# Optimization experiments

Hardware: AMD Instinct MI355X
Metric: run time of the kernel (lower is better)

The kernel has to match this reference:

```python
import jax, jax.numpy as jnp
import numpy as np

V, E, H, L, B, T = 50000, 512, 512, 32, 64, 512


def _lstm_dir(xg, w_hh, reverse):
    # xg: [B,T,4H] precomputed input-to-gate projections (+ biases)
    b, t, g4 = xg.shape
    h_dim = g4 // 4
    def step(carry, xt):
        h, c = carry
        g = xt + h @ w_hh.T  # [B,4H], PyTorch gate order i,f,g,o
        i, f, gg, o = jnp.split(g, 4, axis=-1)
        c = jax.nn.sigmoid(f) * c + jax.nn.sigmoid(i) * jnp.tanh(gg)
        h = jax.nn.sigmoid(o) * jnp.tanh(c)
        return (h, c), h
    init = (jnp.zeros((b, h_dim), xg.dtype), jnp.zeros((b, h_dim), xg.dtype))
    _, hs = jax.lax.scan(step, init, jnp.swapaxes(xg, 0, 1), reverse=reverse)
    return jnp.swapaxes(hs, 0, 1)  # [B,T,H]


def _bilstm(x, w_ih0, w_ih1, w_hh, b_ih, b_hh):
    w_ihs = (w_ih0, w_ih1)
    for l in range(2):
        outs = []
        for d in range(2):  # 0=forward, 1=backward
            xg = jnp.einsum('bti,gi->btg', x, w_ihs[l][d]) + b_ih[l, d] + b_hh[l, d]
            outs.append(_lstm_dir(xg, w_hh[l, d], reverse=(d == 1)))
        x = jnp.concatenate(outs, axis=-1)  # [B,T,2H]
    return x


def _crf_nll(emissions, tags, start, end, trans):
    # pytorch-crf: returns sum log-likelihood; module returns its negation.
    emit = jnp.take_along_axis(emissions, tags[..., None], axis=-1)[..., 0]  # [B,T]
    num = (start[tags[:, 0]] + emit.sum(1)
           + trans[tags[:, :-1], tags[:, 1:]].sum(1) + end[tags[:, -1]])
    alpha0 = start + emissions[:, 0]  # [B,L]
    def step(alpha, e_t):
        s = alpha[:, :, None] + trans[None] + e_t[:, None, :]  # [B,L,L]
        return jax.nn.logsumexp(s, axis=1), None
    alpha, _ = jax.lax.scan(step, alpha0, jnp.swapaxes(emissions[:, 1:], 0, 1))
    denom = jax.nn.logsumexp(alpha + end, axis=-1)  # [B]
    return -(num - denom).sum()


def setup_inputs() -> dict:
    key = jax.random.key(0)
    ks = jax.random.split(key, 13)
    s = 0.05
    emb = jax.random.normal(ks[0], (V, E), jnp.float32) * s
    emb = emb.at[0].set(0.0)  # padding_idx=0
    return {
        'datas': jax.random.randint(ks[1], (B, T), 0, V, jnp.int32),
        'labels': jax.random.randint(ks[2], (B, T), 0, L, jnp.int32),
        'emb': emb,
        'w_ih0': jax.random.normal(ks[3], (2, 4 * H, E), jnp.float32) * s,
        'w_ih1': jax.random.normal(ks[4], (2, 4 * H, 2 * H), jnp.float32) * s,
        'w_hh': jax.random.normal(ks[5], (2, 2, 4 * H, H), jnp.float32) * s,
        'b_ih': jax.random.normal(ks[6], (2, 2, 4 * H), jnp.float32) * s,
        'b_hh': jax.random.normal(ks[7], (2, 2, 4 * H), jnp.float32) * s,
        'w_out': jax.random.normal(ks[8], (2 * H, L), jnp.float32) * s,
        'b_out': jax.random.normal(ks[9], (L,), jnp.float32) * s,
        'crf_start': jax.random.normal(ks[10], (L,), jnp.float32) * s,
        'crf_end': jax.random.normal(ks[11], (L,), jnp.float32) * s,
        'crf_trans': jax.random.normal(ks[12], (L, L), jnp.float32) * s,
    }


def reference(datas, labels, emb, w_ih0, w_ih1, w_hh, b_ih, b_hh, w_out, b_out,
              crf_start, crf_end, crf_trans):
    x = emb[datas]  # [B,T,E]
    h = _bilstm(x, w_ih0, w_ih1, w_hh, b_ih, b_hh)  # [B,T,2H]; dropout=0 (eval)
    emissions = h @ w_out + b_out  # [B,T,L]
    return _crf_nll(emissions, labels, crf_start, crf_end, crf_trans)
```

## Files before the change

### kernel.cpp

```cpp
#include <hip/hip_runtime.h>

typedef unsigned short ushort_t;
typedef unsigned long long u64_t;
typedef __attribute__((ext_vector_type(8))) short short8;
typedef __attribute__((ext_vector_type(4))) float floatx4;


__device__ __forceinline__ float bf2f(ushort_t u) {
  unsigned x = ((unsigned)u) << 16;
  return __builtin_bit_cast(float, x);
}
__device__ __forceinline__ ushort_t f2bf(float f) {
  unsigned x = __builtin_bit_cast(unsigned, f);
  x += 0x7FFFu + ((x >> 16) & 1u);
  return (ushort_t)(x >> 16);
}
__device__ __forceinline__ float sigf(float x) { return 1.0f / (1.0f + __expf(-x)); }
__device__ __forceinline__ float tanhf_(float x) { return 1.0f - 2.0f / (__expf(2.0f * x) + 1.0f); }

static const size_t OFF_A    = 0;
static const size_t OFF_OUT0 = 67108864;
static const size_t OFF_XG   = 134217728;
static const size_t OFF_WIH0 = 167772160;
static const size_t OFF_WIH1 = 171966464;
static const size_t OFF_BIAS = 180355072;
static const size_t OFF_WOUT = 180387840;
static const size_t OFF_HC   = 180453376;
static const size_t OFF_CST  = 181501952;
static const size_t OFF_BAR  = 182026240;
static const size_t OFF_NUM  = 182034432;
static const size_t OFF_PERB = 182034688;
static const size_t OFF_END  = 182034944;

__global__ void prep_kernel(const float* __restrict__ w_ih0, const float* __restrict__ w_ih1,
                            const float* __restrict__ b_ih, const float* __restrict__ b_hh,
                            const float* __restrict__ w_out,
                            ushort_t* __restrict__ wih0_bf, ushort_t* __restrict__ wih1_bf,
                            float* __restrict__ bias, ushort_t* __restrict__ wout_bf) {
  int idx = blockIdx.x * 256 + threadIdx.x;
  int stride = gridDim.x * 256;
  for (int i = idx; i < 2097152; i += stride) wih0_bf[i] = f2bf(w_ih0[i]);
  for (int i = idx; i < 4194304; i += stride) wih1_bf[i] = f2bf(w_ih1[i]);
  for (int i = idx; i < 8192; i += stride) bias[i] = b_ih[i] + b_hh[i];
  for (int i = idx; i < 32768; i += stride) {
    int j = i & 7, Ls = (i >> 3) & 63, kb = (i >> 9) & 31, nt = i >> 14;
    int n = nt * 16 + (Ls & 15);
    int k = kb * 32 + ((Ls >> 4) & 3) * 8 + j;
    wout_bf[i] = f2bf(w_out[k * 32 + n]);
  }
}

__global__ void embed_kernel(const int* __restrict__ datas, const float* __restrict__ emb,
                             ushort_t* __restrict__ x_bf) {
  int idx = blockIdx.x * 256 + threadIdx.x;
  int row = idx >> 6, sub = idx & 63;
  int tok = datas[row];
  const float4* ep = (const float4*)(emb + (size_t)tok * 512 + sub * 8);
  float4 f0 = ep[0], f1 = ep[1];
  short8 v;
  v[0] = (short)f2bf(f0.x); v[1] = (short)f2bf(f0.y);
  v[2] = (short)f2bf(f0.z); v[3] = (short)f2bf(f0.w);
  v[4] = (short)f2bf(f1.x); v[5] = (short)f2bf(f1.y);
  v[6] = (short)f2bf(f1.z); v[7] = (short)f2bf(f1.w);
  *(short8*)(x_bf + (size_t)row * 512 + sub * 8) = v;
}

__global__ __launch_bounds__(256) void gemm_chunk(const ushort_t* __restrict__ A, int K,
                                                  const ushort_t* __restrict__ W,
                                                  const float* __restrict__ biasL,
                                                  ushort_t* __restrict__ xg0c,
                                                  ushort_t* __restrict__ xg1c,
                                                  int t00, int t01) {
  __shared__ alignas(16) ushort_t alds[512 * 8];
  __shared__ alignas(16) ushort_t blds[512 * 8];
  int gid = blockIdx.x;
  int dir = gid >> 9, r = gid & 511;
  int mt = r & 31, ntt = r >> 5;
  int t0 = dir ? t01 : t00;
  const ushort_t* Bm = W + (size_t)dir * 2048 * K;
  const float* bptr = biasL + dir * 2048;
  ushort_t* xg = dir ? xg1c : xg0c;
  int bm0 = mt * 128, bn0 = ntt * 128;
  int tid = threadIdx.x, L = tid & 63, w = tid >> 6;
  int wm = w & 1, wn = w >> 1;
  floatx4 acc[4][4] = {};
  for (int k0 = 0; k0 < K; k0 += 32) {
    __syncthreads();
    #pragma unroll
    for (int rep = 0; rep < 2; rep++) {
      int slot = rep * 256 + tid;
      int t8 = slot >> 6, Ls = slot & 63;
      int col = k0 + (Ls >> 4) * 8;
      int mp = bm0 + t8 * 16 + (Ls & 15);
      int Arow = (mp >> 6) * 512 + t0 + (mp & 63);
      *(short8*)&alds[slot * 8] = *(const short8*)&A[(size_t)Arow * K + col];
      int rowb = bn0 + t8 * 16 + (Ls & 15);
      *(short8*)&blds[slot * 8] = *(const short8*)&Bm[(size_t)rowb * K + col];
    }
    __syncthreads();
    short8 af[4];
    #pragma unroll
    for (int a = 0; a < 4; a++) af[a] = *(const short8*)&alds[((wm * 4 + a) * 64 + L) * 8];
    #pragma unroll
    for (int bq = 0; bq < 4; bq++) {
      short8 bfr = *(const short8*)&blds[((wn * 4 + bq) * 64 + L) * 8];
      #pragma unroll
      for (int a = 0; a < 4; a++)
        acc[a][bq] = __builtin_amdgcn_mfma_f32_16x16x32_bf16(af[a], bfr, acc[a][bq], 0, 0, 0);
    }
  }
  int lm = L >> 4, ln = L & 15;
  #pragma unroll
  for (int bq = 0; bq < 4; bq++) {
    int n = bn0 + (wn * 4 + bq) * 16 + ln;
    float bv = bptr[n];
    #pragma unroll
    for (int a = 0; a < 4; a++) {
      #pragma unroll
      for (int rr = 0; rr < 4; rr++) {
        int m = bm0 + (wm * 4 + a) * 16 + lm * 4 + rr;
        int b = m >> 6, ts = m & 63;
        xg[((size_t)(ts * 64 + b)) * 2048 + n] = f2bf(acc[a][bq][rr] + bv);
      }
    }
  }
}

__global__ __launch_bounds__(256) void lstm_chunk(const ushort_t* __restrict__ xg0c,
                                                  const ushort_t* __restrict__ xg1c,
                                                  const float* __restrict__ whh_f,
                                                  ushort_t* __restrict__ hcL,
                                                  float* __restrict__ cstL,
                                                  ushort_t* __restrict__ outL,
                                                  int* __restrict__ barF, int c) {
  __shared__ alignas(16) ushort_t wlds[32768];
  int bid = blockIdx.x, d = bid >> 5, g = bid & 31, j0 = g * 16;
  int tid = threadIdx.x, L = tid & 63, w = tid >> 6;
  const float* wptr = whh_f + (size_t)d * 2048 * 512;
  #pragma unroll
  for (int it = 0; it < 16; it++) {
    int slot = it * 256 + tid;
    int q = slot >> 10, kb = (slot >> 6) & 15, Ls = slot & 63;
    int gcol = q * 512 + j0 + (Ls & 15);
    int k = kb * 32 + (Ls >> 4) * 8;
    const float* src = wptr + (size_t)gcol * 512 + k;
    float4 f0 = *(const float4*)src;
    float4 f1 = *(const float4*)(src + 4);
    short8 v;
    v[0] = (short)f2bf(f0.x); v[1] = (short)f2bf(f0.y);
    v[2] = (short)f2bf(f0.z); v[3] = (short)f2bf(f0.w);
    v[4] = (short)f2bf(f1.x); v[5] = (short)f2bf(f1.y);
    v[6] = (short)f2bf(f1.z); v[7] = (short)f2bf(f1.w);
    *(short8*)&wlds[slot * 8] = v;
  }
  __syncthreads();
  const ushort_t* xgd = d ? xg1c : xg0c;
  ushort_t* hcd = hcL + (size_t)d * 2 * 32768;
  int* flg = barF + d * 512;
  int* myflag = flg + g * 16;
  int q8 = L >> 4, jj = L & 15;
  int mbase = w * 16 + q8 * 4;
  int wslot = ((w * 16 + (g >> 1)) * 64 + q8 * 4 + 16 * ((g & 1) * 2 + (jj >> 3))) * 8 + (jj & 7);
  int rbase = (w * 16 * 64 + L) * 8;
  float cv[4];
  #pragma unroll
  for (int rr = 0; rr < 4; rr++) cv[rr] = cstL[(size_t)d * 32768 + (mbase + rr) * 512 + j0 + jj];

  auto ldxg = [&](int sl2, ushort_t dst[4][4]) {
    int ts2 = d ? (63 - sl2) : sl2;
    #pragma unroll
    for (int rr = 0; rr < 4; rr++) {
      const ushort_t* xrow = xgd + ((size_t)(ts2 * 64 + mbase + rr)) * 2048 + j0 + jj;
      #pragma unroll
      for (int q = 0; q < 4; q++) dst[q][rr] = xrow[q * 512];
    }
  };

  ushort_t xgu[4][4];
  ldxg(0, xgu);

  for (int sl = 0; sl < 64; sl++) {
    int s = c * 64 + sl;
    int t = d ? (511 - s) : s;
    const u64_t* h64 = (const u64_t*)(hcd + (size_t)(s & 1) * 32768);
    unsigned* h32w = (unsigned*)(hcd + (size_t)((s + 1) & 1) * 32768);
    int b64 = rbase >> 2;
    u64_t hv[32];
    #pragma unroll
    for (int kb = 0; kb < 16; kb++) {
      hv[2 * kb]     = __hip_atomic_load(h64 + b64 + kb * 128,     __ATOMIC_RELAXED, __HIP_MEMORY_SCOPE_SYSTEM);
      hv[2 * kb + 1] = __hip_atomic_load(h64 + b64 + kb * 128 + 1, __ATOMIC_RELAXED, __HIP_MEMORY_SCOPE_SYSTEM);
    }
    floatx4 acc[4] = {};
    #pragma unroll
    for (int kb = 0; kb < 16; kb++) {
      union { u64_t u[2]; short8 v; } pk;
      pk.u[0] = hv[2 * kb];
      pk.u[1] = hv[2 * kb + 1];
      short8 a = pk.v;
      #pragma unroll
      for (int q = 0; q < 4; q++) {
        short8 bfr = *(const short8*)&wlds[((q * 16 + kb) * 64 + L) * 8];
        acc[q] = __builtin_amdgcn_mfma_f32_16x16x32_bf16(a, bfr, acc[q], 0, 0, 0);
      }
    }
    ushort_t hbv[4];
    #pragma unroll
    for (int rr = 0; rr < 4; rr++) {
      float ii = acc[0][rr] + bf2f(xgu[0][rr]);
      float ff = acc[1][rr] + bf2f(xgu[1][rr]);
      float gg = acc[2][rr] + bf2f(xgu[2][rr]);
      float oo = acc[3][rr] + bf2f(xgu[3][rr]);
      float cc = sigf(ff) * cv[rr] + sigf(ii) * tanhf_(gg);
      cv[rr] = cc;
      hbv[rr] = f2bf(sigf(oo) * tanhf_(cc));
    }
    bool evn = (jj & 1) == 0;
    #pragma unroll
    for (int rr = 0; rr < 4; rr++) {
      unsigned mine = (unsigned)hbv[rr];
      unsigned nb = (unsigned)__shfl_xor((int)mine, 1, 64);
      if (evn) {
        unsigned packed = mine | (nb << 16);
        __hip_atomic_store(h32w + ((wslot + rr * 8) >> 1), packed,
                           __ATOMIC_RELAXED, __HIP_MEMORY_SCOPE_SYSTEM);
        int m = mbase + rr;
        *(unsigned*)&outL[((size_t)m * 512 + t) * 1024 + (d << 9) + j0 + jj] = packed;
      }
    }
    if (sl != 63) {
      ldxg(sl + 1, xgu);
      __builtin_amdgcn_s_waitcnt(0);
      __syncthreads();
      if (tid == 0)
        __hip_atomic_store(myflag, s + 1, __ATOMIC_RELAXED, __HIP_MEMORY_SCOPE_SYSTEM);
      if (tid < 64) {
        int target = s + 1, guard = 0;
        while (guard < (1 << 17)) {
          int f = __hip_atomic_load(flg + (tid & 31) * 16, __ATOMIC_RELAXED, __HIP_MEMORY_SCOPE_SYSTEM);
          if (__ballot(f >= target) == ~0ULL) break;
          guard++;
        }
      }
      __syncthreads();
    }
  }
  #pragma unroll
  for (int rr = 0; rr < 4; rr++) cstL[(size_t)d * 32768 + (mbase + rr) * 512 + j0 + jj] = cv[rr];
}

__global__ __launch_bounds__(256) void emis_kernel(const ushort_t* __restrict__ out1,
                                                   const ushort_t* __restrict__ wout_bf,
                                                   const float* __restrict__ b_out,
                                                   float* __restrict__ emis) {
  int tid = threadIdx.x, L = tid & 63, w = tid >> 6;
  int bm0 = blockIdx.x * 128;
  int q8 = L >> 4, ln = L & 15;
  floatx4 acc[2][2] = {};
  #pragma unroll 4
  for (int kb = 0; kb < 32; kb++) {
    short8 a0 = *(const short8*)&out1[(size_t)(bm0 + (w * 2 + 0) * 16 + ln) * 1024 + kb * 32 + q8 * 8];
    short8 a1 = *(const short8*)&out1[(size_t)(bm0 + (w * 2 + 1) * 16 + ln) * 1024 + kb * 32 + q8 * 8];
    #pragma unroll
    for (int nt = 0; nt < 2; nt++) {
      short8 bfr = *(const short8*)&wout_bf[((size_t)(nt * 32 + kb) * 64 + L) * 8];
      acc[0][nt] = __builtin_amdgcn_mfma_f32_16x16x32_bf16(a0, bfr, acc[0][nt], 0, 0, 0);
      acc[1][nt] = __builtin_amdgcn_mfma_f32_16x16x32_bf16(a1, bfr, acc[1][nt], 0, 0, 0);
    }
  }
  #pragma unroll
  for (int mt = 0; mt < 2; mt++) {
    #pragma unroll
    for (int nt = 0; nt < 2; nt++) {
      int n = nt * 16 + ln;
      float bv = b_out[n];
      #pragma unroll
      for (int rr = 0; rr < 4; rr++) {
        int m = bm0 + (w * 2 + mt) * 16 + q8 * 4 + rr;
        emis[(size_t)m * 32 + n] = acc[mt][nt][rr] + bv;
      }
    }
  }
}

__global__ void num_kernel(const int* __restrict__ labels, const float* __restrict__ emis,
                           const float* __restrict__ trans, const float* __restrict__ cstart,
                           const float* __restrict__ cend, float* __restrict__ num) {
  int b = blockIdx.x, tid = threadIdx.x;
  float s = 0.f;
  for (int t = tid; t < 512; t += 64) {
    int tag = labels[b * 512 + t];
    s += emis[(size_t)(b * 512 + t) * 32 + tag];
    if (t < 511) s += trans[tag * 32 + labels[b * 512 + t + 1]];
  }
  #pragma unroll
  for (int off = 32; off > 0; off >>= 1) s += __shfl_xor(s, off, 64);
  if (tid == 0) num[b] = s + cstart[labels[b * 512]] + cend[labels[b * 512 + 511]];
}

__global__ __launch_bounds__(64) void fwd_kernel(const float* __restrict__ emis,
                                                 const float* __restrict__ trans,
                                                 const float* __restrict__ cstart,
                                                 const float* __restrict__ cend,
                                                 const float* __restrict__ num,
                                                 float* __restrict__ perb) {
  int b = blockIdx.x, tid = threadIdx.x, j = tid & 31;
  float trj[32];
  #pragma unroll
  for (int i = 0; i < 32; i++) trj[i] = trans[i * 32 + j];
  float alpha = cstart[j] + emis[(size_t)(b * 512) * 32 + j];
  for (int t = 1; t < 512; t++) {
    float e = emis[(size_t)(b * 512 + t) * 32 + j];
    float m = -1e30f;
    float v[32];
    #pragma unroll
    for (int i = 0; i < 32; i++) {
      v[i] = __shfl(alpha, i, 32) + trj[i];
      m = fmaxf(m, v[i]);
    }
    float s = 0.f;
    #pragma unroll
    for (int i = 0; i < 32; i++) s += __expf(v[i] - m);
    alpha = __logf(s) + m + e;
  }
  float z = alpha + cend[j];
  float m2 = z;
  #pragma unroll
  for (int off = 16; off > 0; off >>= 1) m2 = fmaxf(m2, __shfl_xor(m2, off, 32));
  float s2 = __expf(z - m2);
  #pragma unroll
  for (int off = 16; off > 0; off >>= 1) s2 += __shfl_xor(s2, off, 32);
  if (tid == 0) perb[b] = num[b] - (__logf(s2) + m2);
}

__global__ void final_kernel(const float* __restrict__ perb, float* __restrict__ out) {
  int tid = threadIdx.x;
  float s = perb[tid];
  #pragma unroll
  for (int off = 32; off > 0; off >>= 1) s += __shfl_xor(s, off, 64);
  if (tid == 0) out[0] = -s;
}

extern "C" void kernel_launch(void* const* d_in, const int* in_sizes, int n_in,
                              void* d_out, int out_size, void* d_ws, size_t ws_size,
                              hipStream_t stream) {
  (void)in_sizes; (void)n_in; (void)out_size; (void)ws_size;
  const int* datas = (const int*)d_in[0];
  const int* labels = (const int*)d_in[1];
  const float* emb = (const float*)d_in[2];
  const float* w_ih0 = (const float*)d_in[3];
  const float* w_ih1 = (const float*)d_in[4];
  const float* w_hh = (const float*)d_in[5];
  const float* b_ih = (const float*)d_in[6];
  const float* b_hh = (const float*)d_in[7];
  const float* w_out = (const float*)d_in[8];
  const float* b_out = (const float*)d_in[9];
  const float* cstart = (const float*)d_in[10];
  const float* cend = (const float*)d_in[11];
  const float* ctrans = (const float*)d_in[12];

  char* ws = (char*)d_ws;
  ushort_t* x_bf = (ushort_t*)(ws + OFF_A);
  ushort_t* out1 = (ushort_t*)(ws + OFF_A);
  ushort_t* out0 = (ushort_t*)(ws + OFF_OUT0);
  ushort_t* xg0c = (ushort_t*)(ws + OFF_XG);
  ushort_t* xg1c = (ushort_t*)(ws + OFF_XG + 16777216);
  float* emis = (float*)(ws + OFF_XG);
  ushort_t* wih0_bf = (ushort_t*)(ws + OFF_WIH0);
  ushort_t* wih1_bf = (ushort_t*)(ws + OFF_WIH1);
  float* bias = (float*)(ws + OFF_BIAS);
  ushort_t* wout_bf = (ushort_t*)(ws + OFF_WOUT);
  ushort_t* hc0 = (ushort_t*)(ws + OFF_HC);
  ushort_t* hc1 = hc0 + 131072;
  float* cst0 = (float*)(ws + OFF_CST);
  float* cst1 = cst0 + 65536;
  int* bar = (int*)(ws + OFF_BAR);
  float* numb = (float*)(ws + OFF_NUM);
  float* perb = (float*)(ws + OFF_PERB);

  hipMemsetAsync(ws + OFF_HC, 0, OFF_END - OFF_HC, stream);

  prep_kernel<<<2048, 256, 0, stream>>>(w_ih0, w_ih1, b_ih, b_hh, w_out,
                                        wih0_bf, wih1_bf, bias, wout_bf);
  embed_kernel<<<8192, 256, 0, stream>>>(datas, emb, x_bf);

  for (int c = 0; c < 8; c++) {
    gemm_chunk<<<1024, 256, 0, stream>>>(x_bf, 512, wih0_bf, bias, xg0c, xg1c,
                                         c * 64, (7 - c) * 64);
    lstm_chunk<<<64, 256, 0, stream>>>(xg0c, xg1c, w_hh, hc0, cst0, out0, bar, c);
  }
  for (int c = 0; c < 8; c++) {
    gemm_chunk<<<1024, 256, 0, stream>>>(out0, 1024, wih1_bf, bias + 4096, xg0c, xg1c,
                                         c * 64, (7 - c) * 64);
    lstm_chunk<<<64, 256, 0, stream>>>(xg0c, xg1c, w_hh + 2097152, hc1, cst1, out1,
                                       bar + 1024, c);
  }

  emis_kernel<<<256, 256, 0, stream>>>(out1, wout_bf, b_out, emis);
  num_kernel<<<64, 64, 0, stream>>>(labels, emis, ctrans, cstart, cend, numb);
  fwd_kernel<<<64, 64, 0, stream>>>(emis, ctrans, cstart, cend, numb, perb);
  final_kernel<<<1, 64, 0, stream>>>(perb, (float*)d_out);
}
```

Baseline: 5.757 ms.

## Overlap LSTM output stores with step barrier; exp-domain CRF forward recursion

In the persistent LSTM recurrence kernel, the per-step output writes and the next xg prefetch now happen after the flag publish, overlapping the spin-wait. The full __syncthreads is replaced by a vmcnt wait plus raw s_barrier, which keeps the critical path to only the h-state stores. The CRF forward kernel now computes logsumexp as a max-shifted exp(alpha) dot exp(trans) with precomputed exp(trans), split across four accumulators, and prefetches the next emission. This drops 32 exps per step but relies on exp(trans) staying in range, and the raw barriers need correct memory ordering around the output stores.

```diff
diff --git a/kernel.cpp b/kernel.cpp
--- a/kernel.cpp
+++ b/kernel.cpp
@@ -216,24 +216,30 @@
       hbv[rr] = f2bf(sigf(oo) * tanhf_(cc));
     }
     bool evn = (jj & 1) == 0;
+    unsigned pk4[4];
     #pragma unroll
     for (int rr = 0; rr < 4; rr++) {
       unsigned mine = (unsigned)hbv[rr];
       unsigned nb = (unsigned)__shfl_xor((int)mine, 1, 64);
-      if (evn) {
-        unsigned packed = mine | (nb << 16);
-        __hip_atomic_store(h32w + ((wslot + rr * 8) >> 1), packed,
+      pk4[rr] = mine | (nb << 16);
+      if (evn)
+        __hip_atomic_store(h32w + ((wslot + rr * 8) >> 1), pk4[rr],
                            __ATOMIC_RELAXED, __HIP_MEMORY_SCOPE_SYSTEM);
-        int m = mbase + rr;
-        *(unsigned*)&outL[((size_t)m * 512 + t) * 1024 + (d << 9) + j0 + jj] = packed;
-      }
     }
     if (sl != 63) {
-      ldxg(sl + 1, xgu);
-      __builtin_amdgcn_s_waitcnt(0);
-      __syncthreads();
+      asm volatile("s_waitcnt vmcnt(0)" ::: "memory");
+      __builtin_amdgcn_s_barrier();
+      asm volatile("" ::: "memory");
       if (tid == 0)
         __hip_atomic_store(myflag, s + 1, __ATOMIC_RELAXED, __HIP_MEMORY_SCOPE_SYSTEM);
+      if (evn) {
+        #pragma unroll
+        for (int rr = 0; rr < 4; rr++) {
+          int m = mbase + rr;
+          *(unsigned*)&outL[((size_t)m * 512 + t) * 1024 + (d << 9) + j0 + jj] = pk4[rr];
+        }
+      }
+      ldxg(sl + 1, xgu);
       if (tid < 64) {
         int target = s + 1, guard = 0;
         while (guard < (1 << 17)) {
@@ -242,7 +248,16 @@
           guard++;
         }
       }
-      __syncthreads();
+      __builtin_amdgcn_s_barrier();
+      asm volatile("" ::: "memory");
+    } else {
+      if (evn) {
+        #pragma unroll
+        for (int rr = 0; rr < 4; rr++) {
+          int m = mbase + rr;
+          *(unsigned*)&outL[((size_t)m * 512 + t) * 1024 + (d << 9) + j0 + jj] = pk4[rr];
+        }
+      }
     }
   }
   #pragma unroll
@@ -305,32 +320,39 @@
                                                  const float* __restrict__ num,
                                                  float* __restrict__ perb) {
   int b = blockIdx.x, tid = threadIdx.x, j = tid & 31;
-  float trj[32];
-  #pragma unroll
-  for (int i = 0; i < 32; i++) trj[i] = trans[i * 32 + j];
+  float etr[32];
+  #pragma unroll
+  for (int i = 0; i < 32; i++) etr[i] = __expf(trans[i * 32 + j]);
   float alpha = cstart[j] + emis[(size_t)(b * 512) * 32 + j];
+  float e_cur = emis[(size_t)(b * 512 + 1) * 32 + j];
   for (int t = 1; t < 512; t++) {
-    float e = emis[(size_t)(b * 512 + t) * 32 + j];
-    float m = -1e30f;
-    float v[32];
-    #pragma unroll
-    for (int i = 0; i < 32; i++) {
-      v[i] = __shfl(alpha, i, 32) + trj[i];
-      m = fmaxf(m, v[i]);
-    }
-    float s = 0.f;
-    #pragma unroll
-    for (int i = 0; i < 32; i++) s += __expf(v[i] - m);
-    alpha = __logf(s) + m + e;
+    float e_nx = (t < 511) ? emis[(size_t)(b * 512 + t + 1) * 32 + j] : 0.f;
+    float mA = alpha;
+    mA = fmaxf(mA, __shfl_xor(mA, 1, 32));
+    mA = fmaxf(mA, __shfl_xor(mA, 2, 32));
+    mA = fmaxf(mA, __shfl_xor(mA, 4, 32));
+    mA = fmaxf(mA, __shfl_xor(mA, 8, 32));
+    mA = fmaxf(mA, __shfl_xor(mA, 16, 32));
+    float p = __expf(alpha - mA);
+    float s0 = 0.f, s1 = 0.f, s2 = 0.f, s3 = 0.f;
+    #pragma unroll
+    for (int i = 0; i < 32; i += 4) {
+      s0 = fmaf(__shfl(p, i, 32),     etr[i],     s0);
+      s1 = fmaf(__shfl(p, i + 1, 32), etr[i + 1], s1);
+      s2 = fmaf(__shfl(p, i + 2, 32), etr[i + 2], s2);
+      s3 = fmaf(__shfl(p, i + 3, 32), etr[i + 3], s3);
+    }
+    alpha = __logf((s0 + s1) + (s2 + s3)) + mA + e_cur;
+    e_cur = e_nx;
   }
   float z = alpha + cend[j];
   float m2 = z;
   #pragma unroll
   for (int off = 16; off > 0; off >>= 1) m2 = fmaxf(m2, __shfl_xor(m2, off, 32));
-  float s2 = __expf(z - m2);
-  #pragma unroll
-  for (int off = 16; off > 0; off >>= 1) s2 += __shfl_xor(s2, off, 32);
-  if (tid == 0) perb[b] = num[b] - (__logf(s2) + m2);
+  float s2r = __expf(z - m2);
+  #pragma unroll
+  for (int off = 16; off > 0; off >>= 1) s2r += __shfl_xor(s2r, off, 32);
+  if (tid == 0) perb[b] = num[b] - (__logf(s2r) + m2);
 }
 
 __global__ void final_kernel(const float* __restrict__ perb, float* __restrict__ out) {
```

Measured after the change: 5.449 ms. 5.4% less time.
